# Optimization experiments

Hardware: AMD Instinct MI355X
Metric: run time of the kernel (lower is better)

The kernel has to match this reference:

```python
import jax, jax.numpy as jnp
import numpy as np

SCALE = float(np.sqrt(0.7))


def setup_inputs() -> dict:
    key = jax.random.key(0)
    ks = jax.random.split(key, 8)
    B, H, E, T, S = 8, 512, 256, 2048, 2048
    return {
        "dec_conved": jax.random.normal(ks[0], (B, H, T), dtype=jnp.float32),
        "embedd": jax.random.normal(ks[1], (B, T, E), dtype=jnp.float32),
        "en_conved": jax.random.normal(ks[2], (B, S, E), dtype=jnp.float32),
        "en_combined": jax.random.normal(ks[3], (B, S, E), dtype=jnp.float32),
        # nn.Linear params: W is [out, in], y = x @ W.T + b
        "W_h2e": jax.random.normal(ks[4], (E, H), dtype=jnp.float32) / np.sqrt(H),
        "b_h2e": jax.random.normal(ks[5], (E,), dtype=jnp.float32) * 0.01,
        "W_e2h": jax.random.normal(ks[6], (H, E), dtype=jnp.float32) / np.sqrt(E),
        "b_e2h": jax.random.normal(ks[7], (H,), dtype=jnp.float32) * 0.01,
    }


def reference(dec_conved, embedd, en_conved, en_combined, W_h2e, b_h2e, W_e2h, b_e2h):
    # dec_conved: [B, H, T] -> [B, T, H]
    dc = jnp.swapaxes(dec_conved, 1, 2)
    # hid2emb: [B, T, E]
    dc_emb = jnp.einsum('bth,eh->bte', dc, W_h2e) + b_h2e
    Q = (dc_emb + embedd) * SCALE  # [B, T, E]
    # energy: [B, T, S]
    energy = jnp.einsum('bte,bse->bts', Q, en_conved)
    a = jax.nn.softmax(energy, axis=2)
    # context: [B, T, E]
    context = jnp.einsum('bts,bse->bte', a, en_combined)
    # emb2hid: [B, T, H]
    context = jnp.einsum('bte,he->bth', context, W_e2h) + b_e2h
    conved = (context + dc) * SCALE  # [B, T, H]
    return (a, jnp.swapaxes(conved, 1, 2))
```

## Files before the change

kernel.cpp:

```cpp
#include <hip/hip_runtime.h>
#include <math.h>

#define B_ 8
#define H_ 512
#define E_ 256
#define T_ 2048
#define S_ 2048
static constexpr float SCALE = 0.83666002653407555f;

typedef _Float16 half8 __attribute__((ext_vector_type(8)));
typedef _Float16 half4v __attribute__((ext_vector_type(4)));
typedef float f32x4 __attribute__((ext_vector_type(4)));

__global__ __launch_bounds__(256) void k_cast(const float* __restrict__ in,
                                              _Float16* __restrict__ out, int n8) {
    const int i = blockIdx.x * 256 + threadIdx.x;
    if (i >= n8) return;
    const float4* p = (const float4*)(in + (size_t)i * 8);
    const float4 a = p[0], b = p[1];
    half8 v;
    v[0] = (_Float16)a.x; v[1] = (_Float16)a.y; v[2] = (_Float16)a.z; v[3] = (_Float16)a.w;
    v[4] = (_Float16)b.x; v[5] = (_Float16)b.y; v[6] = (_Float16)b.z; v[7] = (_Float16)b.w;
    *(half8*)(out + (size_t)i * 8) = v;
}

__global__ __launch_bounds__(256) void k_tcast(const float* __restrict__ in,
                                               _Float16* __restrict__ out, int R, int C) {
    __shared__ float tile[32][33];
    const size_t nb = (size_t)R * C;
    const float* inb = in + (size_t)blockIdx.z * nb;
    _Float16* outb = out + (size_t)blockIdx.z * nb;
    const int c0 = blockIdx.x * 32, r0 = blockIdx.y * 32;
    const int tr = threadIdx.x >> 3;
    const int tc = (threadIdx.x & 7) * 4;
    const float4 v = *(const float4*)(inb + (size_t)(r0 + tr) * C + c0 + tc);
    tile[tr][tc + 0] = v.x; tile[tr][tc + 1] = v.y;
    tile[tr][tc + 2] = v.z; tile[tr][tc + 3] = v.w;
    __syncthreads();
    half4v o;
    o[0] = (_Float16)tile[tc + 0][tr]; o[1] = (_Float16)tile[tc + 1][tr];
    o[2] = (_Float16)tile[tc + 2][tr]; o[3] = (_Float16)tile[tc + 3][tr];
    *(half4v*)(outb + (size_t)(c0 + tr) * R + r0 + tc) = o;
}

__device__ __forceinline__ void stage128x32(const _Float16* __restrict__ g, int ld,
                                            _Float16* __restrict__ lds, int tid) {
    const int r = tid >> 2;
    const int c = (tid & 3) * 8;
    const half8 v0 = *(const half8*)(g + (size_t)r * ld + c);
    const half8 v1 = *(const half8*)(g + (size_t)(r + 64) * ld + c);
    *(half8*)(lds + r * 32 + c) = v0;
    *(half8*)(lds + (r + 64) * 32 + c) = v1;
}

__device__ __forceinline__ void stage_f32_128x32(const float* __restrict__ g, int ld,
                                                 _Float16* __restrict__ lds, int tid) {
    const int r = tid >> 1;
    const int c = (tid & 1) * 16;
    const float4* gp = (const float4*)(g + (size_t)r * ld + c);
    const float4 x0 = gp[0], x1 = gp[1], x2 = gp[2], x3 = gp[3];
    half8 v0, v1;
    v0[0] = (_Float16)x0.x; v0[1] = (_Float16)x0.y; v0[2] = (_Float16)x0.z; v0[3] = (_Float16)x0.w;
    v0[4] = (_Float16)x1.x; v0[5] = (_Float16)x1.y; v0[6] = (_Float16)x1.z; v0[7] = (_Float16)x1.w;
    v1[0] = (_Float16)x2.x; v1[1] = (_Float16)x2.y; v1[2] = (_Float16)x2.z; v1[3] = (_Float16)x2.w;
    v1[4] = (_Float16)x3.x; v1[5] = (_Float16)x3.y; v1[6] = (_Float16)x3.z; v1[7] = (_Float16)x3.w;
    *(half8*)(lds + r * 32 + c) = v0;
    *(half8*)(lds + r * 32 + c + 8) = v1;
}

#define MFMA_PROLOG                                                     \
    __shared__ __align__(16) _Float16 Ash[128 * 32];                    \
    __shared__ __align__(16) _Float16 Bsh[128 * 32];                    \
    const int tid = threadIdx.x;                                        \
    const int lane = tid & 63, wv = tid >> 6;                           \
    const int wm = (wv >> 1) * 64, wn = (wv & 1) * 64;                  \
    const int fr = lane & 15, fk = (lane >> 4) * 8;                     \
    f32x4 acc[4][4] = {};

#define MFMA_BODY                                                       \
    half8 af[4], bfr[4];                                                \
    _Pragma("unroll")                                                   \
    for (int i = 0; i < 4; ++i) {                                       \
        af[i]  = *(const half8*)&Ash[(wm + i * 16 + fr) * 32 + fk];     \
        bfr[i] = *(const half8*)&Bsh[(wn + i * 16 + fr) * 32 + fk];     \
    }                                                                   \
    _Pragma("unroll")                                                   \
    for (int mi = 0; mi < 4; ++mi)                                      \
        _Pragma("unroll")                                               \
        for (int ni = 0; ni < 4; ++ni)                                  \
            acc[mi][ni] = __builtin_amdgcn_mfma_f32_16x16x32_f16(       \
                af[mi], bfr[ni], acc[mi][ni], 0, 0, 0);

__global__ __launch_bounds__(256) void k_q_mfma(const _Float16* __restrict__ decT,
                                                const _Float16* __restrict__ W1,
                                                const float* __restrict__ bias,
                                                const float* __restrict__ emb,
                                                _Float16* __restrict__ Qb) {
    MFMA_PROLOG
    const int b = blockIdx.z;
    const int t0 = blockIdx.y * 128;
    const int e0 = blockIdx.x * 128;
    const _Float16* Ab = decT + (size_t)b * T_ * H_ + (size_t)t0 * H_;
    const _Float16* Bb = W1 + (size_t)e0 * H_;
    for (int k0 = 0; k0 < H_; k0 += 32) {
        stage128x32(Ab + k0, H_, Ash, tid);
        stage128x32(Bb + k0, H_, Bsh, tid);
        __syncthreads();
        MFMA_BODY
        __syncthreads();
    }
    const int cr = (lane >> 4) * 4, cn = lane & 15;
    const float* embb = emb + (size_t)b * T_ * E_;
    _Float16* Qo = Qb + (size_t)b * T_ * E_;
#pragma unroll
    for (int mi = 0; mi < 4; ++mi)
#pragma unroll
        for (int r = 0; r < 4; ++r) {
            const int t = t0 + wm + mi * 16 + cr + r;
#pragma unroll
            for (int ni = 0; ni < 4; ++ni) {
                const int e = e0 + wn + ni * 16 + cn;
                const float v = (acc[mi][ni][r] + bias[e] + embb[(size_t)t * E_ + e]) * SCALE;
                Qo[(size_t)t * E_ + e] = (_Float16)v;
            }
        }
}

__global__ __launch_bounds__(256) void k_energy_mfma(const _Float16* __restrict__ Qb,
                                                     const _Float16* __restrict__ Kb,
                                                     float* __restrict__ a_out) {
    MFMA_PROLOG
    const int b = blockIdx.z;
    const int t0 = blockIdx.y * 128;
    const int s0 = blockIdx.x * 128;
    const _Float16* Ab = Qb + (size_t)b * T_ * E_ + (size_t)t0 * E_;
    const _Float16* Bb = Kb + (size_t)b * S_ * E_ + (size_t)s0 * E_;
    for (int k0 = 0; k0 < E_; k0 += 32) {
        stage128x32(Ab + k0, E_, Ash, tid);
        stage128x32(Bb + k0, E_, Bsh, tid);
        __syncthreads();
        MFMA_BODY
        __syncthreads();
    }
    const int cr = (lane >> 4) * 4, cn = lane & 15;
    float* ab = a_out + (size_t)b * T_ * S_;
#pragma unroll
    for (int mi = 0; mi < 4; ++mi)
#pragma unroll
        for (int r = 0; r < 4; ++r) {
            const int t = t0 + wm + mi * 16 + cr + r;
#pragma unroll
            for (int ni = 0; ni < 4; ++ni) {
                const int s = s0 + wn + ni * 16 + cn;
                ab[(size_t)t * S_ + s] = acc[mi][ni][r];
            }
        }
}

__global__ __launch_bounds__(256) void k_softmax(float* __restrict__ a) {
    const size_t row = blockIdx.x;
    float* p = a + row * (size_t)S_;
    float4 v0 = ((const float4*)p)[threadIdx.x];
    float4 v1 = ((const float4*)p)[threadIdx.x + 256];

    float m = fmaxf(fmaxf(fmaxf(v0.x, v0.y), fmaxf(v0.z, v0.w)),
                    fmaxf(fmaxf(v1.x, v1.y), fmaxf(v1.z, v1.w)));
#pragma unroll
    for (int off = 32; off > 0; off >>= 1) m = fmaxf(m, __shfl_down(m, off));
    __shared__ float redm[4];
    __shared__ float reds[4];
    const int wid = threadIdx.x >> 6, lane = threadIdx.x & 63;
    if (lane == 0) redm[wid] = m;
    __syncthreads();
    m = fmaxf(fmaxf(redm[0], redm[1]), fmaxf(redm[2], redm[3]));

    v0.x = __expf(v0.x - m); v0.y = __expf(v0.y - m); v0.z = __expf(v0.z - m); v0.w = __expf(v0.w - m);
    v1.x = __expf(v1.x - m); v1.y = __expf(v1.y - m); v1.z = __expf(v1.z - m); v1.w = __expf(v1.w - m);
    float s = v0.x + v0.y + v0.z + v0.w + v1.x + v1.y + v1.z + v1.w;
#pragma unroll
    for (int off = 32; off > 0; off >>= 1) s += __shfl_down(s, off);
    if (lane == 0) reds[wid] = s;
    __syncthreads();
    s = reds[0] + reds[1] + reds[2] + reds[3];
    const float inv = 1.0f / s;

    v0.x *= inv; v0.y *= inv; v0.z *= inv; v0.w *= inv;
    v1.x *= inv; v1.y *= inv; v1.z *= inv; v1.w *= inv;
    ((float4*)p)[threadIdx.x] = v0;
    ((float4*)p)[threadIdx.x + 256] = v1;
}

__global__ __launch_bounds__(256) void k_ctx_mfma(const float* __restrict__ a,
                                                  const _Float16* __restrict__ Vt,
                                                  _Float16* __restrict__ ctxb) {
    MFMA_PROLOG
    const int b = blockIdx.z;
    const int t0 = blockIdx.y * 128;
    const int e0 = blockIdx.x * 128;
    const float* Ab = a + (size_t)b * T_ * S_ + (size_t)t0 * S_;
    const _Float16* Bb = Vt + (size_t)b * E_ * S_ + (size_t)e0 * S_;
    for (int k0 = 0; k0 < S_; k0 += 32) {
        stage_f32_128x32(Ab + k0, S_, Ash, tid);
        stage128x32(Bb + k0, S_, Bsh, tid);
        __syncthreads();
        MFMA_BODY
        __syncthreads();
    }
    const int cr = (lane >> 4) * 4, cn = lane & 15;
    _Float16* co = ctxb + (size_t)b * T_ * E_;
#pragma unroll
    for (int mi = 0; mi < 4; ++mi)
#pragma unroll
        for (int r = 0; r < 4; ++r) {
            const int t = t0 + wm + mi * 16 + cr + r;
#pragma unroll
            for (int ni = 0; ni < 4; ++ni) {
                const int e = e0 + wn + ni * 16 + cn;
                co[(size_t)t * E_ + e] = (_Float16)acc[mi][ni][r];
            }
        }
}

__global__ __launch_bounds__(256) void k_out_mfma(const _Float16* __restrict__ W2,
                                                  const _Float16* __restrict__ ctxb,
                                                  const float* __restrict__ bias,
                                                  const float* __restrict__ dec,
                                                  float* __restrict__ out2) {
    MFMA_PROLOG
    const int b = blockIdx.z;
    const int h0 = blockIdx.y * 128;
    const int t0 = blockIdx.x * 128;
    const _Float16* Ab = W2 + (size_t)h0 * E_;
    const _Float16* Bb = ctxb + (size_t)b * T_ * E_ + (size_t)t0 * E_;
    for (int k0 = 0; k0 < E_; k0 += 32) {
        stage128x32(Ab + k0, E_, Ash, tid);
        stage128x32(Bb + k0, E_, Bsh, tid);
        __syncthreads();
        MFMA_BODY
        __syncthreads();
    }
    const int cr = (lane >> 4) * 4, cn = lane & 15;
    const float* decb = dec + (size_t)b * H_ * T_;
    float* ob = out2 + (size_t)b * H_ * T_;
#pragma unroll
    for (int mi = 0; mi < 4; ++mi)
#pragma unroll
        for (int r = 0; r < 4; ++r) {
            const int h = h0 + wm + mi * 16 + cr + r;
            const float bj = bias[h];
#pragma unroll
            for (int ni = 0; ni < 4; ++ni) {
                const int t = t0 + wn + ni * 16 + cn;
                const size_t idx = (size_t)h * T_ + t;
                ob[idx] = (acc[mi][ni][r] + bj + decb[idx]) * SCALE;
            }
        }
}

extern "C" void kernel_launch(void* const* d_in, const int* in_sizes, int n_in,
                              void* d_out, int out_size, void* d_ws, size_t ws_size,
                              hipStream_t stream) {
    const float* dec   = (const float*)d_in[0];
    const float* emb   = (const float*)d_in[1];
    const float* enc   = (const float*)d_in[2];
    const float* encc  = (const float*)d_in[3];
    const float* W_h2e = (const float*)d_in[4];
    const float* b_h2e = (const float*)d_in[5];
    const float* W_e2h = (const float*)d_in[6];
    const float* b_e2h = (const float*)d_in[7];

    float* a_out = (float*)d_out;
    float* out2  = a_out + (size_t)B_ * T_ * S_;

    _Float16* ws    = (_Float16*)d_ws;
    _Float16* decT  = ws;
    _Float16* encK  = decT + (size_t)B_ * T_ * H_;
    _Float16* enccT = encK + (size_t)B_ * S_ * E_;
    _Float16* W1b   = enccT + (size_t)B_ * S_ * E_;
    _Float16* W2b   = W1b + (size_t)E_ * H_;
    _Float16* Qb    = W2b + (size_t)H_ * E_;
    _Float16* ctxb  = Qb + (size_t)B_ * T_ * E_;

    const dim3 blk(256);
    k_cast <<<dim3((B_ * S_ * E_ / 8 + 255) / 256), blk, 0, stream>>>(enc, encK, B_ * S_ * E_ / 8);
    k_cast <<<dim3((E_ * H_ / 8 + 255) / 256),      blk, 0, stream>>>(W_h2e, W1b, E_ * H_ / 8);
    k_cast <<<dim3((H_ * E_ / 8 + 255) / 256),      blk, 0, stream>>>(W_e2h, W2b, H_ * E_ / 8);
    k_tcast<<<dim3(T_ / 32, H_ / 32, B_), blk, 0, stream>>>(dec, decT, H_, T_);
    k_tcast<<<dim3(E_ / 32, S_ / 32, B_), blk, 0, stream>>>(encc, enccT, S_, E_);
    k_q_mfma     <<<dim3(E_ / 128, T_ / 128, B_), blk, 0, stream>>>(decT, W1b, b_h2e, emb, Qb);
    k_energy_mfma<<<dim3(S_ / 128, T_ / 128, B_), blk, 0, stream>>>(Qb, encK, a_out);
    k_softmax    <<<dim3(B_ * T_),                blk, 0, stream>>>(a_out);
    k_ctx_mfma   <<<dim3(E_ / 128, T_ / 128, B_), blk, 0, stream>>>(a_out, enccT, ctxb);
    k_out_mfma   <<<dim3(T_ / 128, H_ / 128, B_), blk, 0, stream>>>(W2b, ctxb, b_e2h, dec, out2);
}
```

Baseline: 415.1 us.

## Stage GEMM tiles via global_load_lds, emit fp16 probabilities, shrink Q/ctx tiles

```diff
diff --git a/kernel.cpp b/kernel.cpp
--- a/kernel.cpp
+++ b/kernel.cpp
@@ -1,5 +1,6 @@
 #include <hip/hip_runtime.h>
 #include <math.h>
+#include <stdint.h>
 
 #define B_ 8
 #define H_ 512
@@ -43,29 +44,25 @@
     *(half4v*)(outb + (size_t)(c0 + tr) * R + r0 + tc) = o;
 }
 
-__device__ __forceinline__ void stage128x32(const _Float16* __restrict__ g, int ld,
-                                            _Float16* __restrict__ lds, int tid) {
-    const int r = tid >> 2;
-    const int c = (tid & 3) * 8;
-    const half8 v0 = *(const half8*)(g + (size_t)r * ld + c);
-    const half8 v1 = *(const half8*)(g + (size_t)(r + 64) * ld + c);
-    *(half8*)(lds + r * 32 + c) = v0;
-    *(half8*)(lds + (r + 64) * 32 + c) = v1;
-}
-
-__device__ __forceinline__ void stage_f32_128x32(const float* __restrict__ g, int ld,
-                                                 _Float16* __restrict__ lds, int tid) {
-    const int r = tid >> 1;
-    const int c = (tid & 1) * 16;
-    const float4* gp = (const float4*)(g + (size_t)r * ld + c);
-    const float4 x0 = gp[0], x1 = gp[1], x2 = gp[2], x3 = gp[3];
-    half8 v0, v1;
-    v0[0] = (_Float16)x0.x; v0[1] = (_Float16)x0.y; v0[2] = (_Float16)x0.z; v0[3] = (_Float16)x0.w;
-    v0[4] = (_Float16)x1.x; v0[5] = (_Float16)x1.y; v0[6] = (_Float16)x1.z; v0[7] = (_Float16)x1.w;
-    v1[0] = (_Float16)x2.x; v1[1] = (_Float16)x2.y; v1[2] = (_Float16)x2.z; v1[3] = (_Float16)x2.w;
-    v1[4] = (_Float16)x3.x; v1[5] = (_Float16)x3.y; v1[6] = (_Float16)x3.z; v1[7] = (_Float16)x3.w;
-    *(half8*)(lds + r * 32 + c) = v0;
-    *(half8*)(lds + r * 32 + c + 8) = v1;
+__device__ __forceinline__ void gl_lds16(const _Float16* g, _Float16* l) {
+    __builtin_amdgcn_global_load_lds(
+        (const __attribute__((address_space(1))) void*)g,
+        (__attribute__((address_space(3))) void*)l, 16, 0, 0);
+}
+
+__device__ __forceinline__ void stage128x32_gl(const _Float16* __restrict__ g, int ld,
+                                               _Float16* __restrict__ lds, int wv, int l) {
+    const int r = (wv << 4) + (l >> 2);
+    const int c = (l & 3) << 3;
+    gl_lds16(g + (size_t)r * ld + c, lds + (wv << 9));
+    gl_lds16(g + (size_t)(r + 64) * ld + c, lds + ((wv + 4) << 9));
+}
+
+__device__ __forceinline__ void stage64x32_gl(const _Float16* __restrict__ g, int ld,
+                                              _Float16* __restrict__ lds, int wv, int l) {
+    const int r = (wv << 4) + (l >> 2);
+    const int c = (l & 3) << 3;
+    gl_lds16(g + (size_t)r * ld + c, lds + (wv << 9));
 }
 
 #define MFMA_PROLOG                                                     \
@@ -91,29 +88,53 @@
             acc[mi][ni] = __builtin_amdgcn_mfma_f32_16x16x32_f16(       \
                 af[mi], bfr[ni], acc[mi][ni], 0, 0, 0);
 
+#define MFMA_PROLOG64                                                   \
+    __shared__ __align__(16) _Float16 Ash[64 * 32];                     \
+    __shared__ __align__(16) _Float16 Bsh[128 * 32];                    \
+    const int tid = threadIdx.x;                                        \
+    const int lane = tid & 63, wv = tid >> 6;                           \
+    const int wm = (wv >> 1) * 32, wn = (wv & 1) * 64;                  \
+    const int fr = lane & 15, fk = (lane >> 4) * 8;                     \
+    f32x4 acc[2][4] = {};
+
+#define MFMA_BODY64                                                     \
+    half8 af[2], bfr[4];                                                \
+    _Pragma("unroll")                                                   \
+    for (int i = 0; i < 2; ++i)                                         \
+        af[i]  = *(const half8*)&Ash[(wm + i * 16 + fr) * 32 + fk];     \
+    _Pragma("unroll")                                                   \
+    for (int i = 0; i < 4; ++i)                                         \
+        bfr[i] = *(const half8*)&Bsh[(wn + i * 16 + fr) * 32 + fk];     \
+    _Pragma("unroll")                                                   \
+    for (int mi = 0; mi < 2; ++mi)                                      \
+        _Pragma("unroll")                                               \
+        for (int ni = 0; ni < 4; ++ni)                                  \
+            acc[mi][ni] = __builtin_amdgcn_mfma_f32_16x16x32_f16(       \
+                af[mi], bfr[ni], acc[mi][ni], 0, 0, 0);
+
 __global__ __launch_bounds__(256) void k_q_mfma(const _Float16* __restrict__ decT,
                                                 const _Float16* __restrict__ W1,
                                                 const float* __restrict__ bias,
                                                 const float* __restrict__ emb,
                                                 _Float16* __restrict__ Qb) {
-    MFMA_PROLOG
+    MFMA_PROLOG64
     const int b = blockIdx.z;
-    const int t0 = blockIdx.y * 128;
+    const int t0 = blockIdx.y * 64;
     const int e0 = blockIdx.x * 128;
     const _Float16* Ab = decT + (size_t)b * T_ * H_ + (size_t)t0 * H_;
     const _Float16* Bb = W1 + (size_t)e0 * H_;
     for (int k0 = 0; k0 < H_; k0 += 32) {
-        stage128x32(Ab + k0, H_, Ash, tid);
-        stage128x32(Bb + k0, H_, Bsh, tid);
-        __syncthreads();
-        MFMA_BODY
+        stage64x32_gl(Ab + k0, H_, Ash, wv, lane);
+        stage128x32_gl(Bb + k0, H_, Bsh, wv, lane);
+        __syncthreads();
+        MFMA_BODY64
         __syncthreads();
     }
     const int cr = (lane >> 4) * 4, cn = lane & 15;
     const float* embb = emb + (size_t)b * T_ * E_;
     _Float16* Qo = Qb + (size_t)b * T_ * E_;
 #pragma unroll
-    for (int mi = 0; mi < 4; ++mi)
+    for (int mi = 0; mi < 2; ++mi)
 #pragma unroll
         for (int r = 0; r < 4; ++r) {
             const int t = t0 + wm + mi * 16 + cr + r;
@@ -136,8 +157,8 @@
     const _Float16* Ab = Qb + (size_t)b * T_ * E_ + (size_t)t0 * E_;
     const _Float16* Bb = Kb + (size_t)b * S_ * E_ + (size_t)s0 * E_;
     for (int k0 = 0; k0 < E_; k0 += 32) {
-        stage128x32(Ab + k0, E_, Ash, tid);
-        stage128x32(Bb + k0, E_, Bsh, tid);
+        stage128x32_gl(Ab + k0, E_, Ash, wv, lane);
+        stage128x32_gl(Bb + k0, E_, Bsh, wv, lane);
         __syncthreads();
         MFMA_BODY
         __syncthreads();
@@ -157,7 +178,8 @@
         }
 }
 
-__global__ __launch_bounds__(256) void k_softmax(float* __restrict__ a) {
+__global__ __launch_bounds__(256) void k_softmax(float* __restrict__ a,
+                                                 _Float16* __restrict__ a16) {
     const size_t row = blockIdx.x;
     float* p = a + row * (size_t)S_;
     float4 v0 = ((const float4*)p)[threadIdx.x];
@@ -188,28 +210,35 @@
     v1.x *= inv; v1.y *= inv; v1.z *= inv; v1.w *= inv;
     ((float4*)p)[threadIdx.x] = v0;
     ((float4*)p)[threadIdx.x + 256] = v1;
-}
-
-__global__ __launch_bounds__(256) void k_ctx_mfma(const float* __restrict__ a,
+
+    _Float16* q = a16 + row * (size_t)S_;
+    half4v h0, h1;
+    h0[0] = (_Float16)v0.x; h0[1] = (_Float16)v0.y; h0[2] = (_Float16)v0.z; h0[3] = (_Float16)v0.w;
+    h1[0] = (_Float16)v1.x; h1[1] = (_Float16)v1.y; h1[2] = (_Float16)v1.z; h1[3] = (_Float16)v1.w;
+    *(half4v*)(q + (size_t)threadIdx.x * 4) = h0;
+    *(half4v*)(q + 1024 + (size_t)threadIdx.x * 4) = h1;
+}
+
+__global__ __launch_bounds__(256) void k_ctx_mfma(const _Float16* __restrict__ a16,
                                                   const _Float16* __restrict__ Vt,
                                                   _Float16* __restrict__ ctxb) {
-    MFMA_PROLOG
+    MFMA_PROLOG64
     const int b = blockIdx.z;
-    const int t0 = blockIdx.y * 128;
+    const int t0 = blockIdx.y * 64;
     const int e0 = blockIdx.x * 128;
-    const float* Ab = a + (size_t)b * T_ * S_ + (size_t)t0 * S_;
+    const _Float16* Ab = a16 + (size_t)b * T_ * S_ + (size_t)t0 * S_;
     const _Float16* Bb = Vt + (size_t)b * E_ * S_ + (size_t)e0 * S_;
     for (int k0 = 0; k0 < S_; k0 += 32) {
-        stage_f32_128x32(Ab + k0, S_, Ash, tid);
-        stage128x32(Bb + k0, S_, Bsh, tid);
-        __syncthreads();
-        MFMA_BODY
+        stage64x32_gl(Ab + k0, S_, Ash, wv, lane);
+        stage128x32_gl(Bb + k0, S_, Bsh, wv, lane);
+        __syncthreads();
+        MFMA_BODY64
         __syncthreads();
     }
     const int cr = (lane >> 4) * 4, cn = lane & 15;
     _Float16* co = ctxb + (size_t)b * T_ * E_;
 #pragma unroll
-    for (int mi = 0; mi < 4; ++mi)
+    for (int mi = 0; mi < 2; ++mi)
 #pragma unroll
         for (int r = 0; r < 4; ++r) {
             const int t = t0 + wm + mi * 16 + cr + r;
@@ -233,8 +262,8 @@
     const _Float16* Ab = W2 + (size_t)h0 * E_;
     const _Float16* Bb = ctxb + (size_t)b * T_ * E_ + (size_t)t0 * E_;
     for (int k0 = 0; k0 < E_; k0 += 32) {
-        stage128x32(Ab + k0, E_, Ash, tid);
-        stage128x32(Bb + k0, E_, Bsh, tid);
+        stage128x32_gl(Ab + k0, E_, Ash, wv, lane);
+        stage128x32_gl(Bb + k0, E_, Bsh, wv, lane);
         __syncthreads();
         MFMA_BODY
         __syncthreads();
@@ -280,6 +309,7 @@
     _Float16* W2b   = W1b + (size_t)E_ * H_;
     _Float16* Qb    = W2b + (size_t)H_ * E_;
     _Float16* ctxb  = Qb + (size_t)B_ * T_ * E_;
+    _Float16* a16   = ctxb + (size_t)B_ * T_ * E_;
 
     const dim3 blk(256);
     k_cast <<<dim3((B_ * S_ * E_ / 8 + 255) / 256), blk, 0, stream>>>(enc, encK, B_ * S_ * E_ / 8);
@@ -287,9 +317,9 @@
     k_cast <<<dim3((H_ * E_ / 8 + 255) / 256),      blk, 0, stream>>>(W_e2h, W2b, H_ * E_ / 8);
     k_tcast<<<dim3(T_ / 32, H_ / 32, B_), blk, 0, stream>>>(dec, decT, H_, T_);
     k_tcast<<<dim3(E_ / 32, S_ / 32, B_), blk, 0, stream>>>(encc, enccT, S_, E_);
-    k_q_mfma     <<<dim3(E_ / 128, T_ / 128, B_), blk, 0, stream>>>(decT, W1b, b_h2e, emb, Qb);
+    k_q_mfma     <<<dim3(E_ / 128, T_ / 64, B_),  blk, 0, stream>>>(decT, W1b, b_h2e, emb, Qb);
     k_energy_mfma<<<dim3(S_ / 128, T_ / 128, B_), blk, 0, stream>>>(Qb, encK, a_out);
-    k_softmax    <<<dim3(B_ * T_),                blk, 0, stream>>>(a_out);
-    k_ctx_mfma   <<<dim3(E_ / 128, T_ / 128, B_), blk, 0, stream>>>(a_out, enccT, ctxb);
+    k_softmax    <<<dim3(B_ * T_),                blk, 0, stream>>>(a_out, a16);
+    k_ctx_mfma   <<<dim3(E_ / 128, T_ / 64, B_),  blk, 0, stream>>>(a16, enccT, ctxb);
     k_out_mfma   <<<dim3(T_ / 128, H_ / 128, B_), blk, 0, stream>>>(W2b, ctxb, b_e2h, dec, out2);
 }
```

After: 421.9 us. Within noise of the previous version (+1.6%).
